# Performance work log

Measured on AMD Instinct MI355X. Metric: run time of the kernel, lower is better.

## Reference

```python
import jax, jax.numpy as jnp
import numpy as np

B, S, E, H = 1, 2048, 2048, 16
D = E // H  # head_dim = 128
EPS = 1e-6
NEG_INF = -1e30


def _rms_norm(x, gamma):
    # RMSNorm over last dim: x / sqrt(mean(x^2)+eps) * gamma
    return x * jax.lax.rsqrt(jnp.mean(x * x, axis=-1, keepdims=True) + EPS) * gamma


def _rotate_half(x):
    x1, x2 = jnp.split(x, 2, axis=-1)
    return jnp.concatenate([-x2, x1], axis=-1)


def _rope(x, cos, sin):
    # x: [B,H,S,D]; cos/sin: [S,D] broadcast over batch and heads
    return x * cos + _rotate_half(x) * sin


def setup_inputs() -> dict:
    key = jax.random.key(0)
    ks = jax.random.split(key, 5)
    sc = lambda n: 1.0 / np.sqrt(n)
    x = jax.random.normal(ks[0], (B, S, E), jnp.float32)
    # realistic RoPE tables
    inv_freq = 1.0 / (10000.0 ** (jnp.arange(0, D, 2, dtype=jnp.float32) / D))
    t = jnp.arange(S, dtype=jnp.float32)
    freqs = jnp.outer(t, inv_freq)                    # [S, D/2]
    emb = jnp.concatenate([freqs, freqs], axis=-1)    # [S, D]
    cos, sin = jnp.cos(emb), jnp.sin(emb)
    Wq = jax.random.normal(ks[1], (E, E), jnp.float32) * sc(E)
    Wk = jax.random.normal(ks[2], (D, E), jnp.float32) * sc(E)
    Wv = jax.random.normal(ks[3], (D, E), jnp.float32) * sc(E)
    Wo = jax.random.normal(ks[4], (E, E), jnp.float32) * sc(E)
    q_gamma = jnp.ones((D,), jnp.float32)
    k_gamma = jnp.ones((D,), jnp.float32)
    return dict(x=x, cos=cos, sin=sin, Wq=Wq, Wk=Wk, Wv=Wv, Wo=Wo,
                q_gamma=q_gamma, k_gamma=k_gamma)


def reference(x, cos, sin, Wq, Wk, Wv, Wo, q_gamma, k_gamma):
    # projections (Linear with bias=False -> x @ W.T)
    Q = (x @ Wq.T).reshape(B, S, H, D).transpose(0, 2, 1, 3)  # [B,H,S,D]
    K = (x @ Wk.T)[:, None, :, :]                             # [B,1,S,D]
    V = x @ Wv.T                                              # [B,S,D] (single KV head)
    # qk-norm
    Q = _rms_norm(Q, q_gamma)
    K = _rms_norm(K, k_gamma)  # computed then discarded below (faithful to source)
    # RoPE — source bug replicated: K is overwritten with roped Q
    Q = _rope(Q, cos, sin)
    K = _rope(Q, cos, sin)     # [B,H,S,D]
    # causal attention (dense stand-in for flash_attn_func, scale 1/sqrt(D))
    scores = jnp.einsum('bhqd,bhkd->bhqk', Q, K) / jnp.sqrt(jnp.float32(D))
    causal = jnp.tril(jnp.ones((S, S), bool))
    scores = jnp.where(causal, scores, NEG_INF)
    probs = jax.nn.softmax(scores, axis=-1)
    # single V head broadcast across query heads
    out = jnp.einsum('bhqk,bkd->bqhd', probs, V).reshape(B, S, E)
    return out @ Wo.T
```

## Files before the change

kernel.cpp:

```cpp
#include <hip/hip_runtime.h>
#include <hip/hip_bf16.h>

#define SL 2048
#define NH 16
#define HD 128
#define EMB 2048

typedef __attribute__((ext_vector_type(8))) __bf16 bf16x8;
typedef __attribute__((ext_vector_type(4))) float f32x4;
typedef __attribute__((ext_vector_type(8))) short short8;

__device__ __forceinline__ short bf16bits(float x) {
  union { __hip_bfloat16 h; short s; } u;
  u.h = __float2bfloat16(x);
  return u.s;
}

#define GLDS16(gp, lp) __builtin_amdgcn_global_load_lds( \
    (__attribute__((address_space(1))) void*)(gp), \
    (__attribute__((address_space(3))) void*)(lp), 16, 0, 0)

__global__ __launch_bounds__(256) void cast_f32_bf16(const float* __restrict__ in,
                                                     short* __restrict__ out, int n) {
  int i = (blockIdx.x * 256 + threadIdx.x) * 8;
  if (i >= n) return;
  float4 a = *(const float4*)(in + i);
  float4 b = *(const float4*)(in + i + 4);
  short8 o;
  o[0] = bf16bits(a.x); o[1] = bf16bits(a.y); o[2] = bf16bits(a.z); o[3] = bf16bits(a.w);
  o[4] = bf16bits(b.x); o[5] = bf16bits(b.y); o[6] = bf16bits(b.z); o[7] = bf16bits(b.w);
  *(short8*)(out + i) = o;
}

template<int MODE>
__global__ __launch_bounds__(256, 3) void gemm64(const short* __restrict__ A,
                                                 const short* __restrict__ B,
                                                 float* __restrict__ C,
                                                 short* __restrict__ Qb,
                                                 short* __restrict__ Kb,
                                                 short* __restrict__ VT,
                                                 const float* __restrict__ cosT,
                                                 const float* __restrict__ sinT,
                                                 const float* __restrict__ gamma) {
  __shared__ char lds_raw[36864];
  short* As = (short*)lds_raw;
  short* Bs = (short*)(lds_raw + 12288);
  const int K = 2048;
  int nwg = gridDim.x;
  int id = blockIdx.x;
  int nid = (id & 7) * (nwg >> 3) + (id >> 3);
  int tn = nid >> 5;
  int tm = nid & 31;
  int tid = threadIdx.x;
  int wave = tid >> 6, lane = tid & 63;
  int g = lane >> 4, c = lane & 15;
  int wr = wave >> 1, wc = wave & 1;
  const short* Ab = A + (long)(tm * 64) * K;
  const short* Bb = B + (long)(tn * 128) * K;
  int swz = (lane & 3) ^ ((lane >> 3) & 3);
  int rdc = (g ^ ((c >> 1) & 3)) * 8;
  f32x4 zero = {0.f, 0.f, 0.f, 0.f};
  f32x4 acc[2][4];
#pragma unroll
  for (int m = 0; m < 2; ++m)
#pragma unroll
    for (int n = 0; n < 4; ++n) acc[m][n] = zero;

#define STG(buf, kt) do { \
    GLDS16(Ab + (long)(wave * 16 + (lane >> 2)) * K + (kt) + swz * 8, \
           As + (buf) * 2048 + wave * 512); \
    _Pragma("unroll") \
    for (int hh = 0; hh < 2; ++hh) { \
      int rb = wave * 32 + hh * 16; \
      GLDS16(Bb + (long)(rb + (lane >> 2)) * K + (kt) + swz * 8, \
             Bs + (buf) * 4096 + rb * 32); \
    } } while (0)

  STG(0, 0);
  STG(1, 32);
  asm volatile("s_waitcnt vmcnt(3)" ::: "memory");
  __builtin_amdgcn_s_barrier();

  int b0 = 0, b1 = 1, b2 = 2;
  for (int it = 0; it < 64; ++it) {
    if (it < 62) STG(b2, (it + 2) * 32);
    bf16x8 a[2], b[4];
#pragma unroll
    for (int m = 0; m < 2; ++m)
      a[m] = *(const bf16x8*)(As + b0 * 2048 + (wr * 32 + m * 16 + c) * 32 + rdc);
#pragma unroll
    for (int n = 0; n < 4; ++n)
      b[n] = *(const bf16x8*)(Bs + b0 * 4096 + (wc * 64 + n * 16 + c) * 32 + rdc);
    __builtin_amdgcn_s_setprio(1);
#pragma unroll
    for (int m = 0; m < 2; ++m)
#pragma unroll
      for (int n = 0; n < 4; ++n)
        acc[m][n] = __builtin_amdgcn_mfma_f32_16x16x32_bf16(a[m], b[n], acc[m][n], 0, 0, 0);
    __builtin_amdgcn_s_setprio(0);
    if (it < 62) {
      asm volatile("s_waitcnt vmcnt(3)" ::: "memory");
      __builtin_amdgcn_s_barrier();
    } else if (it == 62) {
      asm volatile("s_waitcnt vmcnt(0)" ::: "memory");
      __builtin_amdgcn_s_barrier();
    }
    int t = b0; b0 = b1; b1 = b2; b2 = t;
  }
#undef STG

  if constexpr (MODE == 0) {
#pragma unroll
    for (int m = 0; m < 2; ++m)
#pragma unroll
      for (int n = 0; n < 4; ++n)
#pragma unroll
        for (int r = 0; r < 4; ++r) {
          int row = tm * 64 + wr * 32 + m * 16 + g * 4 + r;
          int col = tn * 128 + wc * 64 + n * 16 + c;
          C[(long)row * 2048 + col] = acc[m][n][r];
        }
  } else {
    if (tn < 16) {
      __shared__ float ssb[2][64];
      float* xch = (float*)lds_raw;
      float ssmr[2][4];
#pragma unroll
      for (int m = 0; m < 2; ++m)
#pragma unroll
        for (int r = 0; r < 4; ++r) {
          float s = 0.f;
#pragma unroll
          for (int n = 0; n < 4; ++n) s += acc[m][n][r] * acc[m][n][r];
#pragma unroll
          for (int off = 1; off <= 8; off <<= 1) s += __shfl_xor(s, off, 64);
          ssmr[m][r] = s;
        }
      if (c == 0) {
#pragma unroll
        for (int m = 0; m < 2; ++m)
#pragma unroll
          for (int r = 0; r < 4; ++r)
            ssb[wc][wr * 32 + m * 16 + g * 4 + r] = ssmr[m][r];
      }
      __syncthreads();
      float rn[2][4];
#pragma unroll
      for (int m = 0; m < 2; ++m)
#pragma unroll
        for (int r = 0; r < 4; ++r) {
          int rowloc = wr * 32 + m * 16 + g * 4 + r;
          rn[m][r] = rsqrtf((ssb[0][rowloc] + ssb[1][rowloc]) * (1.0f / 128.0f) + 1e-6f);
        }
      float g_own[4], g_par[4];
#pragma unroll
      for (int n = 0; n < 4; ++n) {
        g_own[n] = gamma[wc * 64 + n * 16 + c];
        g_par[n] = gamma[(wc ^ 1) * 64 + n * 16 + c];
      }
      float sgn = wc ? 1.f : -1.f;
#pragma unroll
      for (int m = 0; m < 2; ++m) {
        __syncthreads();
#pragma unroll
        for (int n = 0; n < 4; ++n)
#pragma unroll
          for (int r = 0; r < 4; ++r)
            xch[tid * 17 + n * 4 + r] = acc[m][n][r];
        __syncthreads();
        float xp[4][4];
#pragma unroll
        for (int n = 0; n < 4; ++n)
#pragma unroll
          for (int r = 0; r < 4; ++r)
            xp[n][r] = xch[(tid ^ 64) * 17 + n * 4 + r];
#pragma unroll
        for (int n = 0; n < 4; ++n)
#pragma unroll
          for (int r = 0; r < 4; ++r) {
            int s = tm * 64 + wr * 32 + m * 16 + g * 4 + r;
            int u = n * 16 + c;
            float cv = cosT[s * 128 + u];
            float sv = sinT[s * 128 + u];
            float xo = acc[m][n][r] * rn[m][r] * g_own[n];
            float xq = xp[n][r] * rn[m][r] * g_par[n];
            float y  = xo * cv + sgn * xq * sv;
            float yp = xq * cv - sgn * xo * sv;
            float kk = y * cv + sgn * yp * sv;
            long o = ((long)tn * SL + s) * HD + wc * 64 + u;
            Qb[o] = bf16bits(y);
            Kb[o] = bf16bits(kk);
          }
      }
    } else {
#pragma unroll
      for (int m = 0; m < 2; ++m)
#pragma unroll
        for (int n = 0; n < 4; ++n)
#pragma unroll
          for (int r = 0; r < 4; ++r) {
            int s = tm * 64 + wr * 32 + m * 16 + g * 4 + r;
            int d = wc * 64 + n * 16 + c;
            VT[(long)d * SL + s] = bf16bits(acc[m][n][r]);
          }
    }
  }
}

__global__ __launch_bounds__(256, 2) void attn_part(const short* __restrict__ Qb,
                                                    const short* __restrict__ Kb,
                                                    const short* __restrict__ VTg,
                                                    short* __restrict__ att,
                                                    float* __restrict__ pO,
                                                    float* __restrict__ pml) {
  __shared__ short Ks[2][64 * 128];
  __shared__ short Vs[2][128 * 64];
  __shared__ short Ps[4][16 * 72];
  int wave = threadIdx.x >> 6, lane = threadIdx.x & 63;
  int g = lane >> 4, c = lane & 15;
  int h = blockIdx.y;
  int x = blockIdx.x & 15;
  int cbk = blockIdx.x >> 4;
  const short* Qh = Qb + (long)h * SL * HD;
  const short* Kh = Kb + (long)h * SL * HD;
  f32x4 zero = {0.f, 0.f, 0.f, 0.f};
  const float sc = 0.08838834764831845f;

  int pqt[2], plo[2], pcnt[2], pout[2];
  if (cbk == 0) {
    pqt[0] = x;      plo[0] = 0;      pcnt[0] = x + 1;  pout[0] = 0;
    pqt[1] = 31 - x; plo[1] = 0;      pcnt[1] = 16 - x; pout[1] = 1;
  } else {
    pqt[0] = 31 - x; plo[0] = 16 - x; pcnt[0] = 16;     pout[0] = 2;
    pqt[1] = 0;      plo[1] = 0;      pcnt[1] = 0;      pout[1] = 0;
  }
  int total = pcnt[0] + pcnt[1];

#define ASTAGE(b, kvb) do { \
    _Pragma("unroll") \
    for (int i = 0; i < 4; ++i) { \
      int rb = wave * 16 + i * 4; \
      int row = rb + (lane >> 4); \
      int c16 = (lane & 15) ^ (row & 7); \
      GLDS16(Kh + (long)((kvb) + row) * HD + c16 * 8, &Ks[b][rb * 128]); \
    } \
    _Pragma("unroll") \
    for (int i = 0; i < 4; ++i) { \
      int dbase = i * 32 + wave * 8; \
      int drow = dbase + (lane >> 3); \
      int u8 = (lane & 7) ^ (drow & 7); \
      GLDS16(VTg + (long)drow * SL + (kvb) + u8 * 8, &Vs[b][dbase * 64]); \
    } } while (0)

  ASTAGE(0, plo[0] * 64);
  int s = 0;

  for (int p = 0; p < 2; ++p) {
    int nt = pcnt[p];
    if (nt == 0) break;
    int qt = pqt[p];
    int qb = qt * 64 + wave * 16;
    int qown = qb + c;

    bf16x8 aq[4];
#pragma unroll
    for (int kc = 0; kc < 4; ++kc)
      aq[kc] = *(const bf16x8*)(Qh + (long)qown * HD + kc * 32 + g * 8);

    float m = -1e30f, l = 0.f;
    f32x4 O[8];
#pragma unroll
    for (int d8 = 0; d8 < 8; ++d8) O[d8] = zero;

    for (int i = 0; i < nt; ++i, ++s) {
      int kt = plo[p] + i;
      int kvb = kt * 64;
      int bcu = s & 1;
      asm volatile("s_waitcnt vmcnt(0)" ::: "memory");
      __builtin_amdgcn_s_barrier();
      {
        int ns = s + 1;
        if (ns < total) {
          int np = (ns < pcnt[0]) ? 0 : 1;
          int nkt = plo[np] + (ns - (np ? pcnt[0] : 0));
          ASTAGE(bcu ^ 1, nkt * 64);
        }
      }

      f32x4 sf[4];
#pragma unroll
      for (int n = 0; n < 4; ++n) sf[n] = zero;
      __builtin_amdgcn_s_setprio(1);
#pragma unroll
      for (int kc = 0; kc < 4; ++kc)
#pragma unroll
        for (int n = 0; n < 4; ++n) {
          int row = n * 16 + c;
          int u = (kc * 4 + g) ^ (row & 7);
          bf16x8 bk = *(const bf16x8*)(&Ks[bcu][row * 128 + u * 8]);
          sf[n] = __builtin_amdgcn_mfma_f32_16x16x32_bf16(bk, aq[kc], sf[n], 0, 0, 0);
        }
      __builtin_amdgcn_s_setprio(0);

      float pm = -1e30f;
      if (kt == qt) {
#pragma unroll
        for (int n = 0; n < 4; ++n) {
#pragma unroll
          for (int r = 0; r < 4; ++r) {
            int k = kvb + n * 16 + g * 4 + r;
            float v = sf[n][r] * sc;
            if (k > qown) v = -1e30f;
            sf[n][r] = v;
          }
          float a0 = fmaxf(sf[n][0], sf[n][1]);
          float a1 = fmaxf(sf[n][2], sf[n][3]);
          pm = fmaxf(pm, fmaxf(a0, a1));
        }
      } else {
#pragma unroll
        for (int n = 0; n < 4; ++n) {
#pragma unroll
          for (int r = 0; r < 4; ++r) sf[n][r] *= sc;
          float a0 = fmaxf(sf[n][0], sf[n][1]);
          float a1 = fmaxf(sf[n][2], sf[n][3]);
          pm = fmaxf(pm, fmaxf(a0, a1));
        }
      }
      pm = fmaxf(pm, __shfl_xor(pm, 16, 64));
      pm = fmaxf(pm, __shfl_xor(pm, 32, 64));

      if (__any(pm > m + 8.f)) {
        float mn_ = fmaxf(m, pm);
        float corr = __expf(m - mn_);
        m = mn_;
        l *= corr;
        float c4[4];
#pragma unroll
        for (int r = 0; r < 4; ++r) c4[r] = __shfl(corr, g * 4 + r, 64);
#pragma unroll
        for (int d8 = 0; d8 < 8; ++d8)
#pragma unroll
          for (int r = 0; r < 4; ++r) O[d8][r] *= c4[r];
      }

#pragma unroll
      for (int n = 0; n < 4; ++n)
#pragma unroll
        for (int hh = 0; hh < 2; ++hh) {
          float p0 = __expf(sf[n][2 * hh + 0] - m);
          float p1 = __expf(sf[n][2 * hh + 1] - m);
          l += p0 + p1;
          unsigned pk = (unsigned)(unsigned short)bf16bits(p0) |
                        ((unsigned)(unsigned short)bf16bits(p1) << 16);
          *(unsigned*)&Ps[wave][c * 72 + n * 16 + g * 4 + 2 * hh] = pk;
        }

#pragma unroll
      for (int k2 = 0; k2 < 2; ++k2) {
        bf16x8 ap = *(const bf16x8*)(&Ps[wave][c * 72 + k2 * 32 + g * 8]);
        __builtin_amdgcn_s_setprio(1);
#pragma unroll
        for (int d8 = 0; d8 < 8; ++d8) {
          int drow = d8 * 16 + c;
          int u = (k2 * 4 + g) ^ (c & 7);
          bf16x8 bv = *(const bf16x8*)(&Vs[bcu][drow * 64 + u * 8]);
          O[d8] = __builtin_amdgcn_mfma_f32_16x16x32_bf16(ap, bv, O[d8], 0, 0, 0);
        }
        __builtin_amdgcn_s_setprio(0);
      }
    }

    if (pout[p] == 0) {
      float lf = l;
      lf += __shfl_xor(lf, 16, 64);
      lf += __shfl_xor(lf, 32, 64);
      float rinv = 1.0f / lf;
      float r4[4];
#pragma unroll
      for (int r = 0; r < 4; ++r) r4[r] = __shfl(rinv, g * 4 + r, 64);
#pragma unroll
      for (int d8 = 0; d8 < 8; ++d8)
#pragma unroll
        for (int r = 0; r < 4; ++r) {
          int q = qb + g * 4 + r;
          att[(long)q * EMB + h * HD + d8 * 16 + c] = bf16bits(O[d8][r] * r4[r]);
        }
    } else {
      int part = pout[p] - 1;
      float lf = l;
      lf += __shfl_xor(lf, 16, 64);
      lf += __shfl_xor(lf, 32, 64);
      float* Op = pO + ((long)(part * 16 + x) * 16 + h) * 8192;
#pragma unroll
      for (int d8 = 0; d8 < 8; ++d8)
#pragma unroll
        for (int r = 0; r < 4; ++r)
          Op[(wave * 16 + g * 4 + r) * 128 + d8 * 16 + c] = O[d8][r];
      if (g == 0) {
        float* pmb = pml + ((part * 16 + x) * 16 + h) * 64 + wave * 16 + c;
        pmb[0]     = m;
        pmb[32768] = lf;
      }
    }
  }
#undef ASTAGE
}

__global__ __launch_bounds__(256) void attn_comb(const float* __restrict__ pO,
                                                 const float* __restrict__ pml,
                                                 short* __restrict__ att) {
  int b = blockIdx.x;
  int x = b & 15, h = b >> 4;
  int qt = 31 - x;
  int t = threadIdx.x;
  int q = t >> 2, d0 = (t & 3) * 32;
  int i0 = (x * 16 + h) * 64 + q;
  int i1 = (256 + x * 16 + h) * 64 + q;
  float m0 = pml[i0], m1 = pml[i1];
  float l0 = pml[32768 + i0], l1 = pml[32768 + i1];
  float M = fmaxf(m0, m1);
  float w0 = __expf(m0 - M), w1 = __expf(m1 - M);
  float inv = 1.0f / (l0 * w0 + l1 * w1);
  const float* O0 = pO + ((long)(x * 16 + h)) * 8192 + q * 128 + d0;
  const float* O1 = pO + ((long)(256 + x * 16 + h)) * 8192 + q * 128 + d0;
  short* out = att + (long)(qt * 64 + q) * EMB + h * HD + d0;
#pragma unroll
  for (int j = 0; j < 32; j += 4) {
    float4 a = *(const float4*)(O0 + j);
    float4 bb = *(const float4*)(O1 + j);
    out[j + 0] = bf16bits((a.x * w0 + bb.x * w1) * inv);
    out[j + 1] = bf16bits((a.y * w0 + bb.y * w1) * inv);
    out[j + 2] = bf16bits((a.z * w0 + bb.z * w1) * inv);
    out[j + 3] = bf16bits((a.w * w0 + bb.w * w1) * inv);
  }
}

extern "C" void kernel_launch(void* const* d_in, const int* in_sizes, int n_in,
                              void* d_out, int out_size, void* d_ws, size_t ws_size,
                              hipStream_t stream) {
  const float* x    = (const float*)d_in[0];
  const float* cosT = (const float*)d_in[1];
  const float* sinT = (const float*)d_in[2];
  const float* Wq   = (const float*)d_in[3];
  const float* Wv   = (const float*)d_in[5];
  const float* Wo   = (const float*)d_in[6];
  const float* qg   = (const float*)d_in[7];

  char* w = (char*)d_ws;
  short* xb   = (short*)(w + 0);
  short* wqvb = (short*)(w + 8388608);
  short* wob  = (short*)(w + 17301504);
  short* vt   = (short*)(w + 25690112);
  short* qb   = (short*)(w + 26214400);
  short* kb   = (short*)(w + 34603008);
  short* attb = (short*)(w + 42991616);
  float* pO   = (float*)(w + 0);
  float* pml  = (float*)(w + 16777216);

  cast_f32_bf16<<<dim3(2048), dim3(256), 0, stream>>>(x,  xb,   4194304);
  cast_f32_bf16<<<dim3(2048), dim3(256), 0, stream>>>(Wq, wqvb, 4194304);
  cast_f32_bf16<<<dim3(128),  dim3(256), 0, stream>>>(Wv, wqvb + 4194304, 262144);
  cast_f32_bf16<<<dim3(2048), dim3(256), 0, stream>>>(Wo, wob,  4194304);

  gemm64<1><<<dim3(544), dim3(256), 0, stream>>>(xb, wqvb, nullptr, qb, kb, vt,
                                                 cosT, sinT, qg);
  attn_part<<<dim3(32, 16), dim3(256), 0, stream>>>(qb, kb, vt, attb, pO, pml);
  attn_comb<<<dim3(256), dim3(256), 0, stream>>>(pO, pml, attb);
  gemm64<0><<<dim3(512), dim3(256), 0, stream>>>(attb, wob, (float*)d_out,
                                                 nullptr, nullptr, nullptr,
                                                 nullptr, nullptr, nullptr);
}
```

Before: 137.1 us.

## Use 128x128 tile GEMM with 512 threads for Q projection and output projection

Adds a new 128x128-tile GEMM kernel using 8 waves, a 4-stage global-to-LDS pipeline and a 128KB LDS arena. It is used for the fused Q projection with RMSNorm/RoPE epilogue and for the output projection. The V projection now runs as its own small 64-tile launch. The larger tiles give more data reuse per loaded byte, and the RoPE epilogue needs only a single LDS exchange. In exchange, occupancy drops to one block per CU, there are only 256 blocks, and there is an extra kernel launch.

```diff
diff --git a/kernel.cpp b/kernel.cpp
--- a/kernel.cpp
+++ b/kernel.cpp
@@ -33,15 +33,172 @@
 }
 
 template<int MODE>
+__global__ __launch_bounds__(512, 1) void gemm128(const short* __restrict__ A,
+                                                  const short* __restrict__ B,
+                                                  float* __restrict__ C,
+                                                  short* __restrict__ Qb,
+                                                  short* __restrict__ Kb,
+                                                  const float* __restrict__ cosT,
+                                                  const float* __restrict__ sinT,
+                                                  const float* __restrict__ gamma) {
+  __shared__ char arena[131072];
+  short* As = (short*)arena;
+  const int K = 2048;
+  int id = blockIdx.x;
+  int nid = (id & 7) * 32 + (id >> 3);
+  int tn = nid >> 4, tm = nid & 15;
+  int tid = threadIdx.x;
+  int w = tid >> 6, lane = tid & 63;
+  int g = lane >> 4, c = lane & 15;
+  int wr = w >> 2, wc = w & 3;
+  const short* Ab = A + (long)(tm * 128) * K;
+  const short* Bb = B + (long)(tn * 128) * K;
+  int lr = lane >> 3;
+  int lsw = (lane & 7) ^ lr;
+  f32x4 zero = {0.f, 0.f, 0.f, 0.f};
+  f32x4 acc[4][2];
+#pragma unroll
+  for (int m = 0; m < 4; ++m)
+#pragma unroll
+    for (int n = 0; n < 2; ++n) acc[m][n] = zero;
+
+#define STG(buf, kt) do { \
+    _Pragma("unroll") \
+    for (int j = 0; j < 2; ++j) { \
+      int rb = w * 16 + j * 8; \
+      GLDS16(Ab + (long)(rb + lr) * K + (kt) + lsw * 8, \
+             As + (buf) * 16384 + rb * 64); \
+      GLDS16(Bb + (long)(rb + lr) * K + (kt) + lsw * 8, \
+             As + (buf) * 16384 + 8192 + rb * 64); \
+    } } while (0)
+
+  STG(0, 0);
+  STG(1, 64);
+  STG(2, 128);
+  asm volatile("s_waitcnt vmcnt(8)" ::: "memory");
+  __builtin_amdgcn_s_barrier();
+
+  for (int it = 0; it < 32; ++it) {
+    int bf = it & 3;
+    if (it < 29) STG((it + 3) & 3, (it + 3) * 64);
+    const short* Ax = As + bf * 16384;
+    const short* Bx = Ax + 8192;
+    bf16x8 af[2][4], bfr[2][2];
+#pragma unroll
+    for (int kk = 0; kk < 2; ++kk) {
+      int ch = ((kk * 4 + g) ^ (c & 7)) * 8;
+#pragma unroll
+      for (int m = 0; m < 4; ++m)
+        af[kk][m] = *(const bf16x8*)(Ax + (wr * 64 + m * 16 + c) * 64 + ch);
+#pragma unroll
+      for (int n = 0; n < 2; ++n)
+        bfr[kk][n] = *(const bf16x8*)(Bx + (wc * 32 + n * 16 + c) * 64 + ch);
+    }
+    __builtin_amdgcn_s_setprio(1);
+#pragma unroll
+    for (int kk = 0; kk < 2; ++kk)
+#pragma unroll
+      for (int m = 0; m < 4; ++m)
+#pragma unroll
+        for (int n = 0; n < 2; ++n)
+          acc[m][n] = __builtin_amdgcn_mfma_f32_16x16x32_bf16(af[kk][m], bfr[kk][n],
+                                                              acc[m][n], 0, 0, 0);
+    __builtin_amdgcn_s_setprio(0);
+    if (it < 29) {
+      asm volatile("s_waitcnt vmcnt(8)" ::: "memory");
+    } else if (it == 29) {
+      asm volatile("s_waitcnt vmcnt(4)" ::: "memory");
+    } else if (it == 30) {
+      asm volatile("s_waitcnt vmcnt(0)" ::: "memory");
+    }
+    if (it < 31) __builtin_amdgcn_s_barrier();
+  }
+#undef STG
+
+  if constexpr (MODE == 0) {
+#pragma unroll
+    for (int m = 0; m < 4; ++m)
+#pragma unroll
+      for (int n = 0; n < 2; ++n)
+#pragma unroll
+        for (int r = 0; r < 4; ++r) {
+          int row = tm * 128 + wr * 64 + m * 16 + g * 4 + r;
+          int col = tn * 128 + wc * 32 + n * 16 + c;
+          C[(long)row * 2048 + col] = acc[m][n][r];
+        }
+  } else {
+    float* xch = (float*)arena;
+    float* ssb = (float*)(arena + 65536);
+    float ssmr[4][4];
+#pragma unroll
+    for (int m = 0; m < 4; ++m)
+#pragma unroll
+      for (int r = 0; r < 4; ++r) {
+        float s = acc[m][0][r] * acc[m][0][r] + acc[m][1][r] * acc[m][1][r];
+#pragma unroll
+        for (int off = 1; off <= 8; off <<= 1) s += __shfl_xor(s, off, 64);
+        ssmr[m][r] = s;
+      }
+    if (c == 0) {
+#pragma unroll
+      for (int m = 0; m < 4; ++m)
+#pragma unroll
+        for (int r = 0; r < 4; ++r)
+          ssb[wc * 128 + wr * 64 + m * 16 + g * 4 + r] = ssmr[m][r];
+    }
+#pragma unroll
+    for (int m = 0; m < 4; ++m)
+#pragma unroll
+      for (int n = 0; n < 2; ++n)
+#pragma unroll
+        for (int r = 0; r < 4; ++r)
+          xch[(wr * 64 + m * 16 + g * 4 + r) * 128 + wc * 32 + n * 16 + c] = acc[m][n][r];
+    __syncthreads();
+    float rn[4][4];
+#pragma unroll
+    for (int m = 0; m < 4; ++m)
+#pragma unroll
+      for (int r = 0; r < 4; ++r) {
+        int rl = wr * 64 + m * 16 + g * 4 + r;
+        float s4 = ssb[rl] + ssb[128 + rl] + ssb[256 + rl] + ssb[384 + rl];
+        rn[m][r] = rsqrtf(s4 * (1.0f / 128.0f) + 1e-6f);
+      }
+    float sgn = (wc < 2) ? -1.f : 1.f;
+    float g_own[2], g_par[2];
+#pragma unroll
+    for (int n = 0; n < 2; ++n) {
+      int d = wc * 32 + n * 16 + c;
+      g_own[n] = gamma[d];
+      g_par[n] = gamma[d ^ 64];
+    }
+#pragma unroll
+    for (int m = 0; m < 4; ++m)
+#pragma unroll
+      for (int n = 0; n < 2; ++n)
+#pragma unroll
+        for (int r = 0; r < 4; ++r) {
+          int rl = wr * 64 + m * 16 + g * 4 + r;
+          int s = tm * 128 + rl;
+          int d = wc * 32 + n * 16 + c;
+          int u = (wc & 1) * 32 + n * 16 + c;
+          float cv = cosT[s * 128 + u];
+          float sv = sinT[s * 128 + u];
+          float xo = acc[m][n][r] * rn[m][r] * g_own[n];
+          float xq = xch[rl * 128 + (d ^ 64)] * rn[m][r] * g_par[n];
+          float y  = xo * cv + sgn * xq * sv;
+          float yp = xq * cv - sgn * xo * sv;
+          float kk = y * cv + sgn * yp * sv;
+          long o = ((long)tn * SL + s) * HD + d;
+          Qb[o] = bf16bits(y);
+          Kb[o] = bf16bits(kk);
+        }
+  }
+}
+
+template<int MODE>
 __global__ __launch_bounds__(256, 3) void gemm64(const short* __restrict__ A,
                                                  const short* __restrict__ B,
-                                                 float* __restrict__ C,
-                                                 short* __restrict__ Qb,
-                                                 short* __restrict__ Kb,
-                                                 short* __restrict__ VT,
-                                                 const float* __restrict__ cosT,
-                                                 const float* __restrict__ sinT,
-                                                 const float* __restrict__ gamma) {
+                                                 short* __restrict__ VT) {
   __shared__ char lds_raw[36864];
   short* As = (short*)lds_raw;
   short* Bs = (short*)(lds_raw + 12288);
@@ -49,7 +206,7 @@
   int nwg = gridDim.x;
   int id = blockIdx.x;
   int nid = (id & 7) * (nwg >> 3) + (id >> 3);
-  int tn = nid >> 5;
+  int tn = 16;
   int tm = nid & 31;
   int tid = threadIdx.x;
   int wave = tid >> 6, lane = tid & 63;
@@ -109,102 +266,16 @@
   }
 #undef STG
 
-  if constexpr (MODE == 0) {
-#pragma unroll
-    for (int m = 0; m < 2; ++m)
-#pragma unroll
-      for (int n = 0; n < 4; ++n)
-#pragma unroll
-        for (int r = 0; r < 4; ++r) {
-          int row = tm * 64 + wr * 32 + m * 16 + g * 4 + r;
-          int col = tn * 128 + wc * 64 + n * 16 + c;
-          C[(long)row * 2048 + col] = acc[m][n][r];
-        }
-  } else {
-    if (tn < 16) {
-      __shared__ float ssb[2][64];
-      float* xch = (float*)lds_raw;
-      float ssmr[2][4];
-#pragma unroll
-      for (int m = 0; m < 2; ++m)
-#pragma unroll
-        for (int r = 0; r < 4; ++r) {
-          float s = 0.f;
-#pragma unroll
-          for (int n = 0; n < 4; ++n) s += acc[m][n][r] * acc[m][n][r];
-#pragma unroll
-          for (int off = 1; off <= 8; off <<= 1) s += __shfl_xor(s, off, 64);
-          ssmr[m][r] = s;
-        }
-      if (c == 0) {
-#pragma unroll
-        for (int m = 0; m < 2; ++m)
-#pragma unroll
-          for (int r = 0; r < 4; ++r)
-            ssb[wc][wr * 32 + m * 16 + g * 4 + r] = ssmr[m][r];
-      }
-      __syncthreads();
-      float rn[2][4];
-#pragma unroll
-      for (int m = 0; m < 2; ++m)
-#pragma unroll
-        for (int r = 0; r < 4; ++r) {
-          int rowloc = wr * 32 + m * 16 + g * 4 + r;
-          rn[m][r] = rsqrtf((ssb[0][rowloc] + ssb[1][rowloc]) * (1.0f / 128.0f) + 1e-6f);
-        }
-      float g_own[4], g_par[4];
-#pragma unroll
-      for (int n = 0; n < 4; ++n) {
-        g_own[n] = gamma[wc * 64 + n * 16 + c];
-        g_par[n] = gamma[(wc ^ 1) * 64 + n * 16 + c];
-      }
-      float sgn = wc ? 1.f : -1.f;
-#pragma unroll
-      for (int m = 0; m < 2; ++m) {
-        __syncthreads();
-#pragma unroll
-        for (int n = 0; n < 4; ++n)
-#pragma unroll
-          for (int r = 0; r < 4; ++r)
-            xch[tid * 17 + n * 4 + r] = acc[m][n][r];
-        __syncthreads();
-        float xp[4][4];
-#pragma unroll
-        for (int n = 0; n < 4; ++n)
-#pragma unroll
-          for (int r = 0; r < 4; ++r)
-            xp[n][r] = xch[(tid ^ 64) * 17 + n * 4 + r];
-#pragma unroll
-        for (int n = 0; n < 4; ++n)
-#pragma unroll
-          for (int r = 0; r < 4; ++r) {
-            int s = tm * 64 + wr * 32 + m * 16 + g * 4 + r;
-            int u = n * 16 + c;
-            float cv = cosT[s * 128 + u];
-            float sv = sinT[s * 128 + u];
-            float xo = acc[m][n][r] * rn[m][r] * g_own[n];
-            float xq = xp[n][r] * rn[m][r] * g_par[n];
-            float y  = xo * cv + sgn * xq * sv;
-            float yp = xq * cv - sgn * xo * sv;
-            float kk = y * cv + sgn * yp * sv;
-            long o = ((long)tn * SL + s) * HD + wc * 64 + u;
-            Qb[o] = bf16bits(y);
-            Kb[o] = bf16bits(kk);
-          }
-      }
-    } else {
-#pragma unroll
-      for (int m = 0; m < 2; ++m)
-#pragma unroll
-        for (int n = 0; n < 4; ++n)
-#pragma unroll
-          for (int r = 0; r < 4; ++r) {
-            int s = tm * 64 + wr * 32 + m * 16 + g * 4 + r;
-            int d = wc * 64 + n * 16 + c;
-            VT[(long)d * SL + s] = bf16bits(acc[m][n][r]);
-          }
-    }
-  }
+#pragma unroll
+  for (int m = 0; m < 2; ++m)
+#pragma unroll
+    for (int n = 0; n < 4; ++n)
+#pragma unroll
+      for (int r = 0; r < 4; ++r) {
+        int s = tm * 64 + wr * 32 + m * 16 + g * 4 + r;
+        int d = wc * 64 + n * 16 + c;
+        VT[(long)d * SL + s] = bf16bits(acc[m][n][r]);
+      }
 }
 
 __global__ __launch_bounds__(256, 2) void attn_part(const short* __restrict__ Qb,
@@ -463,11 +534,12 @@
   cast_f32_bf16<<<dim3(128),  dim3(256), 0, stream>>>(Wv, wqvb + 4194304, 262144);
   cast_f32_bf16<<<dim3(2048), dim3(256), 0, stream>>>(Wo, wob,  4194304);
 
-  gemm64<1><<<dim3(544), dim3(256), 0, stream>>>(xb, wqvb, nullptr, qb, kb, vt,
-                                                 cosT, sinT, qg);
+  gemm128<1><<<dim3(256), dim3(512), 0, stream>>>(xb, wqvb, nullptr, qb, kb,
+                                                  cosT, sinT, qg);
+  gemm64<2><<<dim3(32), dim3(256), 0, stream>>>(xb, wqvb, vt);
   attn_part<<<dim3(32, 16), dim3(256), 0, stream>>>(qb, kb, vt, attb, pO, pml);
   attn_comb<<<dim3(256), dim3(256), 0, stream>>>(pO, pml, attb);
-  gemm64<0><<<dim3(512), dim3(256), 0, stream>>>(attb, wob, (float*)d_out,
-                                                 nullptr, nullptr, nullptr,
-                                                 nullptr, nullptr, nullptr);
-}
+  gemm128<0><<<dim3(256), dim3(512), 0, stream>>>(attb, wob, (float*)d_out,
+                                                  nullptr, nullptr,
+                                                  nullptr, nullptr, nullptr);
+}
```

Result: no change. 136.3 us (-0.6%).
